# Kernel optimization log

Measured on AMD Instinct MI355X. Metric: run time of the kernel, lower is better.

The kernel has to match this reference:

```python
import jax, jax.numpy as jnp
import numpy as np

B, T, D = 4, 2048, 2048
H = 16
Q_RANK, KV_RANK = 1536, 512
NOPE, ROPE_D, V_D = 128, 64, 128
QK_D = NOPE + ROPE_D  # 192
D_FF = 8192
EPS = 1e-6
THETA = 10000.0
SCALE = QK_D ** -0.5  # mscale = 1 (no rope_scaling)


def _w(key, shape):
    fan_in = shape[0]
    return jax.random.normal(key, shape, dtype=jnp.float32) / np.sqrt(fan_in)


def setup_inputs() -> dict:
    key = jax.random.key(0)
    ks = jax.random.split(key, 16)
    return {
        "x": jax.random.normal(ks[0], (B, T, D), dtype=jnp.float32),
        "ln1_w": jnp.ones((D,), jnp.float32),
        "wq_a": _w(ks[1], (D, Q_RANK)),
        "q_a_ln_w": jnp.ones((Q_RANK,), jnp.float32),
        "wq_b": _w(ks[2], (Q_RANK, H * QK_D)),
        "wkv_a": _w(ks[3], (D, KV_RANK + ROPE_D)),
        "kv_a_ln_w": jnp.ones((KV_RANK,), jnp.float32),
        "wkv_b": _w(ks[4], (KV_RANK, H * (NOPE + V_D))),
        "wo": _w(ks[5], (H * V_D, D)),
        "ln2_w": jnp.ones((D,), jnp.float32),
        "w_gate": _w(ks[6], (D, D_FF)),
        "w_up": _w(ks[7], (D, D_FF)),
        "w_down": _w(ks[8], (D_FF, D)),
        "attention_mask": jnp.ones((B, T), jnp.int32),
        "positions": jnp.broadcast_to(jnp.arange(T, dtype=jnp.int32), (B, T)),
    }


def rmsnorm(x, w):
    return x * jax.lax.rsqrt(jnp.mean(x * x, axis=-1, keepdims=True) + EPS) * w


def apply_rope(x, positions):
    # x: [B, T, h, d], positions: [B, T]
    d = x.shape[-1]
    inv_freq = 1.0 / (THETA ** (jnp.arange(0, d, 2, dtype=jnp.float32) / d))
    ang = positions.astype(jnp.float32)[:, :, None] * inv_freq  # [B,T,d/2]
    cos = jnp.cos(ang)[:, :, None, :]
    sin = jnp.sin(ang)[:, :, None, :]
    x1, x2 = jnp.split(x, 2, axis=-1)
    return jnp.concatenate([x1 * cos - x2 * sin, x2 * cos + x1 * sin], axis=-1)


def reference(x, ln1_w, wq_a, q_a_ln_w, wq_b, wkv_a, kv_a_ln_w, wkv_b, wo,
              ln2_w, w_gate, w_up, w_down, attention_mask, positions):
    # --- MLA attention block ---
    h = rmsnorm(x, ln1_w)
    # low-rank q projection
    q = rmsnorm(h @ wq_a, q_a_ln_w) @ wq_b            # [B,T,H*192]
    q = q.reshape(B, T, H, QK_D)
    q_pass, q_rot = jnp.split(q, [NOPE], axis=-1)
    # compressed kv + shared rope key
    ckv = h @ wkv_a                                    # [B,T,512+64]
    k_c, k_rot = jnp.split(ckv, [KV_RANK], axis=-1)
    k_rot = k_rot.reshape(B, T, 1, ROPE_D)
    kv = rmsnorm(k_c, kv_a_ln_w) @ wkv_b               # [B,T,H*(128+128)]
    kv = kv.reshape(B, T, H, NOPE + V_D)
    k_pass, v = jnp.split(kv, [NOPE], axis=-1)
    # split RoPE on rope dims only
    q_rot = apply_rope(q_rot, positions)
    k_rot = jnp.broadcast_to(apply_rope(k_rot, positions), (B, T, H, ROPE_D))
    qh = jnp.concatenate([q_pass, q_rot], axis=-1)     # [B,T,H,192]
    kh = jnp.concatenate([k_pass, k_rot], axis=-1)     # [B,T,H,192]
    # attention with causal + padding mask (V pad-to-192 then slice is a no-op mathematically)
    scores = jnp.einsum('bqhd,bkhd->bhqk', qh, kh) * SCALE
    causal = jnp.tril(jnp.ones((T, T), bool))
    mask = causal[None, None] & attention_mask[:, None, None, :].astype(bool)
    scores = jnp.where(mask, scores, jnp.finfo(scores.dtype).min)
    attn = jax.nn.softmax(scores, axis=-1)
    o = jnp.einsum('bhqk,bkhd->bqhd', attn, v).reshape(B, T, H * V_D)
    x = x + o @ wo
    # --- MLP block ---
    h2 = rmsnorm(x, ln2_w)
    mlp = (jax.nn.silu(h2 @ w_gate) * (h2 @ w_up)) @ w_down
    return x + mlp
```

## Files before the change

kernel.cpp:

```cpp
#include <hip/hip_runtime.h>

typedef float f32x4 __attribute__((ext_vector_type(4)));
typedef __bf16 bf16x8 __attribute__((ext_vector_type(8)));
typedef unsigned short u16x8 __attribute__((ext_vector_type(8)));
typedef unsigned short u16x4 __attribute__((ext_vector_type(4)));

static __device__ __forceinline__ unsigned short f2b(float f) {
  union { float f; unsigned u; } v; v.f = f;
  unsigned r = v.u + 0x7fffu + ((v.u >> 16) & 1u);
  return (unsigned short)(r >> 16);
}
static __device__ __forceinline__ float b2f(unsigned short s) {
  union { unsigned u; float f; } v; v.u = ((unsigned)s) << 16;
  return v.f;
}
static __device__ __forceinline__ void gload_lds16(const unsigned short* g, unsigned short* l) {
  __builtin_amdgcn_global_load_lds((const __attribute__((address_space(1))) void*)g,
                                   (__attribute__((address_space(3))) void*)l, 16, 0, 0);
}

#define NEG_BIG -3.0e38f

__global__ __launch_bounds__(256) void fill_sentinel(float* __restrict__ out, int n, float v) {
  int i = blockIdx.x * 256 + threadIdx.x;
  if (i < n) out[i] = v;
}

__global__ __launch_bounds__(256) void transpose_convert(const float* __restrict__ in,
                                                         unsigned short* __restrict__ out,
                                                         int K, int N, int in_ld, int row0, int col0,
                                                         float scale) {
  __shared__ float tile[32][33];
  const int k0 = blockIdx.y * 32, n0 = blockIdx.x * 32;
  const int tx = threadIdx.x & 31, ty = threadIdx.x >> 5;
#pragma unroll
  for (int i = 0; i < 32; i += 8) {
    int k = k0 + ty + i, n = n0 + tx;
    tile[ty + i][tx] = (k < K && n < N) ? in[(size_t)(row0 + k) * in_ld + col0 + n] : 0.f;
  }
  __syncthreads();
#pragma unroll
  for (int i = 0; i < 32; i += 8) {
    int n = n0 + ty + i, k = k0 + tx;
    if (n < N && k < K) out[(size_t)n * K + k] = f2b(tile[tx][ty + i] * scale);
  }
}

__global__ __launch_bounds__(256) void rmsnorm_kernel(const float* __restrict__ in,
                                                      const float* __restrict__ w,
                                                      unsigned short* __restrict__ out,
                                                      int ncols, int in_stride, int out_stride) {
  const int row = blockIdx.x;
  const float* rp = in + (size_t)row * in_stride;
  const int n4 = ncols >> 2;
  float4 v[2];
  int nv = 0;
  float ss = 0.f;
  for (int c = threadIdx.x; c < n4; c += 256) {
    float4 xv = reinterpret_cast<const float4*>(rp)[c];
    v[nv++] = xv;
    ss += xv.x * xv.x + xv.y * xv.y + xv.z * xv.z + xv.w * xv.w;
  }
#pragma unroll
  for (int m = 32; m; m >>= 1) ss += __shfl_xor(ss, m);
  __shared__ float red[4];
  if ((threadIdx.x & 63) == 0) red[threadIdx.x >> 6] = ss;
  __syncthreads();
  const float total = red[0] + red[1] + red[2] + red[3];
  const float scale = rsqrtf(total / (float)ncols + 1e-6f);
  nv = 0;
  unsigned short* op = out + (size_t)row * out_stride;
  for (int c = threadIdx.x; c < n4; c += 256) {
    float4 xv = v[nv++];
    float4 wv = reinterpret_cast<const float4*>(w)[c];
    u16x4 o;
    o[0] = f2b(xv.x * scale * wv.x);
    o[1] = f2b(xv.y * scale * wv.y);
    o[2] = f2b(xv.z * scale * wv.z);
    o[3] = f2b(xv.w * scale * wv.w);
    reinterpret_cast<u16x4*>(op)[c] = o;
  }
}

__global__ __launch_bounds__(256) void rmsnorm_b16(const unsigned short* __restrict__ in,
                                                   const float* __restrict__ w,
                                                   unsigned short* __restrict__ out,
                                                   int ncols) {
  const int row = blockIdx.x;
  const unsigned short* rp = in + (size_t)row * ncols;
  const int n4 = ncols >> 2;
  float4 v[2];
  int nv = 0;
  float ss = 0.f;
  for (int c = threadIdx.x; c < n4; c += 256) {
    u16x4 xb = reinterpret_cast<const u16x4*>(rp)[c];
    float4 xv = make_float4(b2f(xb[0]), b2f(xb[1]), b2f(xb[2]), b2f(xb[3]));
    v[nv++] = xv;
    ss += xv.x * xv.x + xv.y * xv.y + xv.z * xv.z + xv.w * xv.w;
  }
#pragma unroll
  for (int m = 32; m; m >>= 1) ss += __shfl_xor(ss, m);
  __shared__ float red[4];
  if ((threadIdx.x & 63) == 0) red[threadIdx.x >> 6] = ss;
  __syncthreads();
  const float total = red[0] + red[1] + red[2] + red[3];
  const float scale = rsqrtf(total / (float)ncols + 1e-6f);
  nv = 0;
  unsigned short* op = out + (size_t)row * ncols;
  for (int c = threadIdx.x; c < n4; c += 256) {
    float4 xv = v[nv++];
    float4 wv = reinterpret_cast<const float4*>(w)[c];
    u16x4 o;
    o[0] = f2b(xv.x * scale * wv.x);
    o[1] = f2b(xv.y * scale * wv.y);
    o[2] = f2b(xv.z * scale * wv.z);
    o[3] = f2b(xv.w * scale * wv.w);
    reinterpret_cast<u16x4*>(op)[c] = o;
  }
}

template <int EPI>
__global__ __launch_bounds__(256) void gemm_bt(const unsigned short* __restrict__ A,
                                               const unsigned short* __restrict__ Bt,
                                               float* __restrict__ outf,
                                               unsigned short* __restrict__ outb,
                                               const float* __restrict__ res,
                                               const unsigned short* __restrict__ aux,
                                               int M, int N, int K) {
  __shared__ __align__(16) unsigned short As[128 * 32];
  __shared__ __align__(16) unsigned short Bs[128 * 32];
  const int tid = threadIdx.x;
  const int l = tid & 63;
  const int lr = l & 15, lg = l >> 4;
  const int wr = tid >> 7, wc = (tid >> 6) & 1;

  const int gx = gridDim.x;
  const int nwg = gx * gridDim.y;
  int lin = blockIdx.y * gx + blockIdx.x;
  {
    const int qq = nwg >> 3, rr = nwg & 7;
    const int xcd = lin & 7, idx = lin >> 3;
    lin = (xcd < rr ? xcd * (qq + 1) : rr * (qq + 1) + (xcd - rr) * qq) + idx;
  }
  const int m0 = (lin / gx) * 128, n0 = (lin % gx) * 128;

  f32x4 acc[4][4] = {};

  for (int k0 = 0; k0 < K; k0 += 32) {
#pragma unroll
    for (int j = 0; j < 2; ++j) {
      const int chunk = j * 256 + tid;
      const int row = chunk >> 2, kc = chunk & 3;
      const unsigned short* ga = A + (size_t)(m0 + row) * K + k0 + kc * 8;
      gload_lds16(ga, &As[(size_t)(j * 256 + (tid & 192)) * 8]);
      int rb = n0 + row;
      if (rb > N - 1) rb = N - 1;
      const unsigned short* gb = Bt + (size_t)rb * K + k0 + kc * 8;
      gload_lds16(gb, &Bs[(size_t)(j * 256 + (tid & 192)) * 8]);
    }
    __syncthreads();
    bf16x8 af[4], bfr[4];
#pragma unroll
    for (int mi = 0; mi < 4; ++mi)
      af[mi] = *reinterpret_cast<const bf16x8*>(&As[(wr * 64 + mi * 16 + lr) * 32 + lg * 8]);
#pragma unroll
    for (int ni = 0; ni < 4; ++ni)
      bfr[ni] = *reinterpret_cast<const bf16x8*>(&Bs[(wc * 64 + ni * 16 + lr) * 32 + lg * 8]);
#pragma unroll
    for (int mi = 0; mi < 4; ++mi)
#pragma unroll
      for (int ni = 0; ni < 4; ++ni)
        acc[mi][ni] = __builtin_amdgcn_mfma_f32_16x16x32_bf16(af[mi], bfr[ni], acc[mi][ni], 0, 0, 0);
    __syncthreads();
  }

#pragma unroll
  for (int mi = 0; mi < 4; ++mi) {
#pragma unroll
    for (int ni = 0; ni < 4; ++ni) {
      const int r0 = m0 + wr * 64 + mi * 16 + lg * 4;
      const int c = n0 + wc * 64 + ni * 16 + lr;
      if (c < N) {
#pragma unroll
        for (int j = 0; j < 4; ++j) {
          const size_t idx = (size_t)(r0 + j) * N + c;
          const float v = acc[mi][ni][j];
          if constexpr (EPI == 0) outf[idx] = v;
          else if constexpr (EPI == 1) outb[idx] = f2b(v);
          else if constexpr (EPI == 2) outf[idx] = v + res[idx];
          else if constexpr (EPI == 3) outb[idx] = f2b(v / (1.f + __expf(-v)));
          else outb[idx] = f2b(v * b2f(aux[idx]));
        }
      }
    }
  }
}

template <int EPI>
__global__ __launch_bounds__(512, 1) void gemm256(const unsigned short* __restrict__ A,
                                                  const unsigned short* __restrict__ Bt,
                                                  float* __restrict__ outf,
                                                  unsigned short* __restrict__ outb,
                                                  const float* __restrict__ res,
                                                  const unsigned short* __restrict__ aux,
                                                  int M, int N, int K) {
  __shared__ __align__(16) unsigned short Lds[2][2][2][128 * 64];
  const int tid = threadIdx.x;
  const int l = tid & 63, lr = l & 15, lg = l >> 4;
  const int w = tid >> 6, swr = w >> 2, swn = w & 3;

  const int gn = N >> 8;
  int lin = blockIdx.x;
  {
    const int nwg = gridDim.x;
    lin = (lin & 7) * (nwg >> 3) + (lin >> 3);
  }
  const int npg = gn << 3;
  const int gid = lin / npg;
  const int idx = lin - gid * npg;
  const int m0 = (gid * 8 + (idx & 7)) * 256;
  const int n0 = (idx >> 3) * 256;

  const int NT = K >> 6;

  f32x4 acc[4][8] = {};

  auto stageh = [&](int mat, int rh, int t) {
    const unsigned short* src = mat ? Bt : A;
    const int rbase = (mat ? n0 : m0) + rh * 128;
    const int d = t & 1;
#pragma unroll
    for (int g = 0; g < 2; ++g) {
      const int c = g * 512 + tid;
      const int row = c >> 3;
      const int kc = (c & 7) ^ (row & 7);
      gload_lds16(src + (size_t)(rbase + row) * K + t * 64 + kc * 8,
                  &Lds[d][mat][rh][(size_t)(g * 512 + (tid & ~63)) * 8]);
    }
  };

  stageh(0, 0, 0); stageh(1, 0, 0); stageh(0, 1, 0); stageh(1, 1, 0);
  if (NT > 1) {
    stageh(0, 0, 1); stageh(1, 0, 1);
    asm volatile("s_waitcnt vmcnt(4)" ::: "memory");
  } else {
    asm volatile("s_waitcnt vmcnt(0)" ::: "memory");
  }
  __builtin_amdgcn_s_barrier();
  __builtin_amdgcn_sched_barrier(0);

#define RD_A(qr, fi, kk)                                                                    \
  af[fi][kk] = *reinterpret_cast<const bf16x8*>(                                            \
      &Lds[d][0][qr][(swr * 64 + (fi) * 16 + lr) * 64 + (((kk) * 4 + lg) ^ (lr & 7)) * 8])
#define RD_B(qc, fj, kk)                                                                    \
  bfv[fj][kk] = *reinterpret_cast<const bf16x8*>(                                           \
      &Lds[d][1][qc][(swn * 32 + (fj) * 16 + lr) * 64 + (((kk) * 4 + lg) ^ (lr & 7)) * 8])
#define MFMAQ(q)                                                                            \
  _Pragma("unroll") for (int fi = 0; fi < 4; ++fi)                                          \
  _Pragma("unroll") for (int fj = 0; fj < 2; ++fj)                                          \
  _Pragma("unroll") for (int kk = 0; kk < 2; ++kk)                                          \
      acc[q][fi * 2 + fj] =                                                                 \
          __builtin_amdgcn_mfma_f32_16x16x32_bf16(af[fi][kk], bfv[fj][kk], acc[q][fi * 2 + fj], 0, 0, 0)

  for (int T = 0; T < NT; ++T) {
    const int d = T & 1;
    bf16x8 af[4][2], bfv[2][2];

    RD_A(0, 0, 0); RD_A(0, 0, 1); RD_A(0, 1, 0); RD_A(0, 1, 1);
    RD_A(0, 2, 0); RD_A(0, 2, 1); RD_A(0, 3, 0); RD_A(0, 3, 1);
    RD_B(0, 0, 0); RD_B(0, 0, 1); RD_B(0, 1, 0); RD_B(0, 1, 1);
    if (T + 1 < NT) stageh(0, 1, T + 1);
    __builtin_amdgcn_s_setprio(1);
    MFMAQ(0);
    __builtin_amdgcn_s_setprio(0);
    if (T + 1 < NT) asm volatile("s_waitcnt vmcnt(6)" ::: "memory");
    else            asm volatile("s_waitcnt vmcnt(0)" ::: "memory");
    __builtin_amdgcn_s_barrier();
    __builtin_amdgcn_sched_barrier(0);

    RD_B(1, 0, 0); RD_B(1, 0, 1); RD_B(1, 1, 0); RD_B(1, 1, 1);
    if (T + 1 < NT) stageh(1, 1, T + 1);
    __builtin_amdgcn_s_setprio(1);
    MFMAQ(1);
    __builtin_amdgcn_s_setprio(0);
    __builtin_amdgcn_s_barrier();
    __builtin_amdgcn_sched_barrier(0);

    RD_A(1, 0, 0); RD_A(1, 0, 1); RD_A(1, 1, 0); RD_A(1, 1, 1);
    RD_A(1, 2, 0); RD_A(1, 2, 1); RD_A(1, 3, 0); RD_A(1, 3, 1);
    RD_B(0, 0, 0); RD_B(0, 0, 1); RD_B(0, 1, 0); RD_B(0, 1, 1);
    if (T + 2 < NT) stageh(0, 0, T + 2);
    __builtin_amdgcn_s_setprio(1);
    MFMAQ(2);
    __builtin_amdgcn_s_setprio(0);
    __builtin_amdgcn_s_barrier();
    __builtin_amdgcn_sched_barrier(0);

    RD_B(1, 0, 0); RD_B(1, 0, 1); RD_B(1, 1, 0); RD_B(1, 1, 1);
    if (T + 2 < NT) stageh(1, 0, T + 2);
    __builtin_amdgcn_s_setprio(1);
    MFMAQ(3);
    __builtin_amdgcn_s_setprio(0);
    if (T + 2 < NT)      asm volatile("s_waitcnt vmcnt(8)" ::: "memory");
    else if (T + 1 < NT) asm volatile("s_waitcnt vmcnt(4)" ::: "memory");
    __builtin_amdgcn_s_barrier();
    __builtin_amdgcn_sched_barrier(0);
  }

#undef RD_A
#undef RD_B
#undef MFMAQ

#pragma unroll
  for (int q = 0; q < 4; ++q) {
    const int qr = q >> 1, qc = q & 1;
#pragma unroll
    for (int fi = 0; fi < 4; ++fi) {
#pragma unroll
      for (int fj = 0; fj < 2; ++fj) {
        const int r = m0 + qr * 128 + swr * 64 + fi * 16 + lg * 4;
        const int c = n0 + qc * 128 + swn * 32 + fj * 16 + lr;
#pragma unroll
        for (int j = 0; j < 4; ++j) {
          const size_t idx2 = (size_t)(r + j) * N + c;
          const float v = acc[q][fi * 2 + fj][j];
          if constexpr (EPI == 0) outf[idx2] = v;
          else if constexpr (EPI == 1) outb[idx2] = f2b(v);
          else if constexpr (EPI == 2) outf[idx2] = v + res[idx2];
          else if constexpr (EPI == 3) outb[idx2] = f2b(v / (1.f + __expf(-v)));
          else outb[idx2] = f2b(v * b2f(aux[idx2]));
        }
      }
    }
  }
}

__global__ __launch_bounds__(256) void rope_q(unsigned short* __restrict__ q,
                                              const int* __restrict__ positions) {
  const int row = blockIdx.x;
  const int pos = positions[row];
  unsigned short* qp = q + (size_t)row * 3072;
  const int tid = threadIdx.x;
#pragma unroll
  for (int i = 0; i < 2; ++i) {
    int e = i * 256 + tid;
    int hh = e >> 5, j = e & 31;
    int base = hh * 192 + 128;
    float x1 = b2f(qp[base + j]), x2 = b2f(qp[base + 32 + j]);
    float freq = __expf(-(float)j * (9.210340371976184f / 32.f));
    float sa, ca;
    __sincosf((float)pos * freq, &sa, &ca);
    qp[base + j] = f2b(x1 * ca - x2 * sa);
    qp[base + 32 + j] = f2b(x2 * ca + x1 * sa);
  }
}

__global__ __launch_bounds__(256) void repack_k(const unsigned short* __restrict__ kv,
                                                const float* __restrict__ ckv,
                                                const int* __restrict__ positions,
                                                unsigned short* __restrict__ kh) {
  const int row = blockIdx.x;
  const int tid = threadIdx.x;
  {
    const int hh = tid >> 4, db = tid & 15;
    u16x8 v = *reinterpret_cast<const u16x8*>(kv + (size_t)row * 4096 + hh * 256 + db * 8);
    *reinterpret_cast<u16x8*>(kh + (size_t)row * 3072 + hh * 192 + db * 8) = v;
  }
  __shared__ float o1[32], o2[32];
  if (tid < 32) {
    const int j = tid;
    float x1 = ckv[(size_t)row * 576 + 512 + j];
    float x2 = ckv[(size_t)row * 576 + 544 + j];
    const int pos = positions[row];
    float freq = __expf(-(float)j * (9.210340371976184f / 32.f));
    float sa, ca;
    __sincosf((float)pos * freq, &sa, &ca);
    o1[j] = x1 * ca - x2 * sa;
    o2[j] = x2 * ca + x1 * sa;
  }
  __syncthreads();
#pragma unroll
  for (int i = 0; i < 4; ++i) {
    int e = i * 256 + tid;
    int hh = e >> 6, d = e & 63;
    float v = (d < 32) ? o1[d] : o2[d - 32];
    kh[(size_t)row * 3072 + hh * 192 + 128 + d] = f2b(v);
  }
}

__global__ __launch_bounds__(512) void mla_attn(const unsigned short* __restrict__ qh,
                                                const unsigned short* __restrict__ kh,
                                                const unsigned short* __restrict__ kv,
                                                unsigned short* __restrict__ o) {
  const int T = 2048, H = 16;
  const int bx = blockIdx.x;
  const int b = blockIdx.y >> 4;
  const int h = blockIdx.y & 15;
  const int tid = threadIdx.x, w = tid >> 6, l = tid & 63;
  const int lg = l >> 4, lr = l & 15;

  __shared__ __align__(16) unsigned short Ks[64 * 200];
  __shared__ __align__(16) unsigned short Vts[128 * 64];
  __shared__ __align__(16) unsigned short Pl[8][16 * 72];
  __shared__ float exs[8][16];

  int krow[3], kcol[3];
#pragma unroll
  for (int i = 0; i < 3; ++i) { int c = i * 512 + tid; krow[i] = c / 24; kcol[i] = (c % 24) * 8; }
  const int vkvp = tid >> 4;
  const int vf0 = (tid & 15) * 8;

  const unsigned short* kbase0 = kh + (((size_t)b * T) * H + h) * 192;
  const unsigned short* vbase0 = kv + (((size_t)b * T) * H + h) * 256 + 128;

  bf16x8 ones;
#pragma unroll
  for (int e = 0; e < 8; ++e) ones[e] = (__bf16)1.0f;

  for (int half = 0; half < 2; ++half) {
    const int qt = half ? (15 - bx) : bx;

    bf16x8 qa[6];
    {
      const size_t qrow = (size_t)b * T + qt * 128 + w * 16 + lr;
      const unsigned short* qp = qh + (qrow * H + h) * 192 + lg * 8;
#pragma unroll
      for (int kc = 0; kc < 6; ++kc)
        qa[kc] = *reinterpret_cast<const bf16x8*>(qp + kc * 32);
    }

    u16x8 kreg[3], vregA, vregB;
#pragma unroll
    for (int i = 0; i < 3; ++i)
      kreg[i] = *reinterpret_cast<const u16x8*>(kbase0 + (size_t)krow[i] * 3072 + kcol[i]);
    vregA = *reinterpret_cast<const u16x8*>(vbase0 + (size_t)(2 * vkvp) * 4096 + vf0);
    vregB = *reinterpret_cast<const u16x8*>(vbase0 + (size_t)(2 * vkvp + 1) * 4096 + vf0);

    f32x4 ot[8] = {};
    f32x4 lacc = {};
    float mrow[4] = {NEG_BIG, NEG_BIG, NEG_BIG, NEG_BIG};

    const int ktmax = 2 * qt + 1;
    for (int kt = 0; kt <= ktmax; ++kt) {
#pragma unroll
      for (int i = 0; i < 3; ++i)
        *reinterpret_cast<u16x8*>(&Ks[krow[i] * 200 + kcol[i]]) = kreg[i];
      {
        const int c7 = (vf0 >> 3) & 7;
#pragma unroll
        for (int e = 0; e < 8; ++e) {
          const int blk = (vkvp >> 2) ^ (e ^ c7);
          const unsigned val = (unsigned)(unsigned short)vregA[e] |
                               ((unsigned)(unsigned short)vregB[e] << 16);
          *reinterpret_cast<unsigned*>(&Vts[(vf0 + e) * 64 + blk * 8 + (vkvp & 3) * 2]) = val;
        }
      }
      __syncthreads();

      if (kt < ktmax) {
        const unsigned short* kb = kbase0 + (size_t)(kt + 1) * 64 * 3072;
        const unsigned short* vb = vbase0 + (size_t)(kt + 1) * 64 * 4096;
#pragma unroll
        for (int i = 0; i < 3; ++i)
          kreg[i] = *reinterpret_cast<const u16x8*>(kb + (size_t)krow[i] * 3072 + kcol[i]);
        vregA = *reinterpret_cast<const u16x8*>(vb + (size_t)(2 * vkvp) * 4096 + vf0);
        vregB = *reinterpret_cast<const u16x8*>(vb + (size_t)(2 * vkvp + 1) * 4096 + vf0);
      }

      f32x4 s4[4];
#pragma unroll
      for (int ni = 0; ni < 4; ++ni) {
        f32x4 a = {};
#pragma unroll
        for (int kc = 0; kc < 6; ++kc) {
          bf16x8 kf = *reinterpret_cast<const bf16x8*>(&Ks[(ni * 16 + lr) * 200 + kc * 32 + lg * 8]);
          a = __builtin_amdgcn_mfma_f32_16x16x32_bf16(qa[kc], kf, a, 0, 0, 0);
        }
        s4[ni] = a;
      }
      if (kt >= 2 * qt) {
#pragma unroll
        for (int ni = 0; ni < 4; ++ni) {
          const int colr = ni * 16 + lr;
#pragma unroll
          for (int j = 0; j < 4; ++j) {
            const int qrl = qt * 128 + w * 16 + lg * 4 + j - kt * 64;
            if (colr > qrl) s4[ni][j] = NEG_BIG;
          }
        }
      }

      float pmj[4];
      int need = 0;
#pragma unroll
      for (int j = 0; j < 4; ++j) {
        pmj[j] = fmaxf(fmaxf(s4[0][j], s4[1][j]), fmaxf(s4[2][j], s4[3][j]));
        need |= (pmj[j] > mrow[j] + 8.f) ? 1 : 0;
      }
      if (__any(need)) {
        float al[4];
#pragma unroll
        for (int j = 0; j < 4; ++j) {
          float rm = pmj[j];
#pragma unroll
          for (int m = 1; m < 16; m <<= 1) rm = fmaxf(rm, __shfl_xor(rm, m));
          const float mn = fmaxf(mrow[j], rm);
          al[j] = __expf(mrow[j] - mn);
          mrow[j] = mn;
        }
        if (lr == 0) {
#pragma unroll
          for (int j = 0; j < 4; ++j) exs[w][lg * 4 + j] = al[j];
        }
        const float af = exs[w][lr];
#pragma unroll
        for (int mi = 0; mi < 8; ++mi) {
          ot[mi][0] *= af; ot[mi][1] *= af; ot[mi][2] *= af; ot[mi][3] *= af;
        }
        lacc[0] *= af; lacc[1] *= af; lacc[2] *= af; lacc[3] *= af;
      }

#pragma unroll
      for (int ni = 0; ni < 4; ++ni)
#pragma unroll
        for (int j = 0; j < 4; ++j)
          Pl[w][(lg * 4 + j) * 72 + ni * 16 + lr] = f2b(__expf(s4[ni][j] - mrow[j]));

      bf16x8 pf0 = *reinterpret_cast<const bf16x8*>(&Pl[w][lr * 72 + lg * 8]);
      bf16x8 pf1 = *reinterpret_cast<const bf16x8*>(&Pl[w][lr * 72 + 32 + lg * 8]);
      lacc = __builtin_amdgcn_mfma_f32_16x16x32_bf16(ones, pf0, lacc, 0, 0, 0);
      lacc = __builtin_amdgcn_mfma_f32_16x16x32_bf16(ones, pf1, lacc, 0, 0, 0);
#pragma unroll
      for (int mi = 0; mi < 8; ++mi) {
        const int f = mi * 16 + lr;
        const int sfz = (f & 7) ^ ((f >> 3) & 7);
        const int blk0 = lg ^ sfz;
        const int blk1 = (4 + lg) ^ sfz;
        bf16x8 vf0r = *reinterpret_cast<const bf16x8*>(&Vts[f * 64 + blk0 * 8]);
        ot[mi] = __builtin_amdgcn_mfma_f32_16x16x32_bf16(vf0r, pf0, ot[mi], 0, 0, 0);
        bf16x8 vf1r = *reinterpret_cast<const bf16x8*>(&Vts[f * 64 + blk1 * 8]);
        ot[mi] = __builtin_amdgcn_mfma_f32_16x16x32_bf16(vf1r, pf1, ot[mi], 0, 0, 0);
      }
      __syncthreads();
    }

    const float li = 1.f / lacc[0];
    const size_t orow = (size_t)b * T + qt * 128 + w * 16 + lr;
#pragma unroll
    for (int mi = 0; mi < 8; ++mi)
#pragma unroll
      for (int j = 0; j < 4; ++j) {
        const int feat = mi * 16 + lg * 4 + j;
        o[orow * 2048 + h * 128 + feat] = f2b(ot[mi][j] * li);
      }
  }
}

extern "C" void kernel_launch(void* const* d_in, const int* in_sizes, int n_in,
                              void* d_out, int out_size, void* d_ws, size_t ws_size,
                              hipStream_t stream) {
  (void)in_sizes; (void)n_in;
  const float* x      = (const float*)d_in[0];
  const float* ln1_w  = (const float*)d_in[1];
  const float* wq_a   = (const float*)d_in[2];
  const float* qaln_w = (const float*)d_in[3];
  const float* wq_b   = (const float*)d_in[4];
  const float* wkv_a  = (const float*)d_in[5];
  const float* kvln_w = (const float*)d_in[6];
  const float* wkv_b  = (const float*)d_in[7];
  const float* wo     = (const float*)d_in[8];
  const float* ln2_w  = (const float*)d_in[9];
  const float* w_gate = (const float*)d_in[10];
  const float* w_up   = (const float*)d_in[11];
  const float* w_down = (const float*)d_in[12];
  const int*   pos    = (const int*)d_in[14];
  float* out = (float*)d_out;

  const int Mt = 8192;

  char* ws = (char*)d_ws;
  const size_t R1 = 0;
  const size_t R2 = R1 + 67108864;
  const size_t R3 = R2 + 50331648;
  const size_t R4 = R3 + 50331648;
  const size_t R5 = R4 + 33554432;
  const size_t R6 = R5 + 18874368;
  const size_t REQ = R6 + 9437184;

  if (ws_size < REQ) {
    fill_sentinel<<<dim3((out_size + 255) / 256), dim3(256), 0, stream>>>(
        out, out_size, (float)(ws_size >> 20));
    return;
  }

  unsigned short* qa_b16 = (unsigned short*)(ws + R1);
  unsigned short* kvbuf  = (unsigned short*)(ws + R1);
  unsigned short* qbuf   = (unsigned short*)(ws + R2);
  unsigned short* qan    = (unsigned short*)(ws + R3);
  unsigned short* ckvn   = (unsigned short*)(ws + R3);
  unsigned short* khbuf  = (unsigned short*)(ws + R3);
  unsigned short* hbuf   = (unsigned short*)(ws + R4);
  unsigned short* obuf   = (unsigned short*)(ws + R4);
  float*          ckv    = (float*)(ws + R5);
  unsigned short* slotW  = (unsigned short*)(ws + R6);
  unsigned short* actb  = (unsigned short*)(ws + 0);
  unsigned short* h2b   = (unsigned short*)(ws + 134217728);
  unsigned short* wsl2  = (unsigned short*)(ws + 167772160);

  dim3 blk(256);
  dim3 blk5(512);
  auto tcf = [&](const float* W, int K, int N, float scale) {
    transpose_convert<<<dim3((N + 31) / 32, (K + 31) / 32), blk, 0, stream>>>(W, slotW, K, N, N, 0, 0, scale);
  };
  auto g256 = [&](auto epi, const unsigned short* Aa, const unsigned short* Bb, float* of,
                  unsigned short* ob, const float* rs, const unsigned short* ax, int N, int K) {
    gemm256<decltype(epi)::value><<<dim3(32 * (N >> 8)), blk5, 0, stream>>>(Aa, Bb, of, ob, rs, ax, Mt, N, K);
  };

  rmsnorm_kernel<<<Mt, blk, 0, stream>>>(x, ln1_w, hbuf, 2048, 2048, 2048);
  tcf(wq_a, 2048, 1536, 1.0f);
  g256(std::integral_constant<int,1>{}, hbuf, slotW, nullptr, qa_b16, nullptr, nullptr, 1536, 2048);
  rmsnorm_b16<<<Mt, blk, 0, stream>>>(qa_b16, qaln_w, qan, 1536);
  tcf(wq_b, 1536, 3072, 0.07216878364870322f);
  g256(std::integral_constant<int,1>{}, qan, slotW, nullptr, qbuf, nullptr, nullptr, 3072, 1536);
  tcf(wkv_a, 2048, 576, 1.0f);
  gemm_bt<0><<<dim3(5, 64), blk, 0, stream>>>(hbuf, slotW, ckv, nullptr, nullptr, nullptr, Mt, 576, 2048);
  rmsnorm_kernel<<<Mt, blk, 0, stream>>>(ckv, kvln_w, ckvn, 512, 576, 512);
  tcf(wkv_b, 512, 4096, 1.0f);
  g256(std::integral_constant<int,1>{}, ckvn, slotW, nullptr, kvbuf, nullptr, nullptr, 4096, 512);
  rope_q<<<Mt, blk, 0, stream>>>(qbuf, pos);
  repack_k<<<Mt, blk, 0, stream>>>(kvbuf, ckv, pos, khbuf);
  mla_attn<<<dim3(8, 64), blk5, 0, stream>>>(qbuf, khbuf, kvbuf, obuf);
  tcf(wo, 2048, 2048, 1.0f);
  g256(std::integral_constant<int,2>{}, obuf, slotW, out, nullptr, x, nullptr, 2048, 2048);
  rmsnorm_kernel<<<Mt, blk, 0, stream>>>(out, ln2_w, h2b, 2048, 2048, 2048);
  transpose_convert<<<dim3(256, 64), blk, 0, stream>>>(w_gate, wsl2, 2048, 8192, 8192, 0, 0, 1.0f);
  g256(std::integral_constant<int,3>{}, h2b, wsl2, nullptr, actb, nullptr, nullptr, 8192, 2048);
  transpose_convert<<<dim3(256, 64), blk, 0, stream>>>(w_up, wsl2, 2048, 8192, 8192, 0, 0, 1.0f);
  g256(std::integral_constant<int,4>{}, h2b, wsl2, nullptr, actb, nullptr, actb, 8192, 2048);
  transpose_convert<<<dim3(64, 256), blk, 0, stream>>>(w_down, wsl2, 8192, 2048, 2048, 0, 0, 1.0f);
  g256(std::integral_constant<int,2>{}, actb, wsl2, out, nullptr, out, nullptr, 2048, 8192);
}
```

Before: 1.486 ms.

## Fuse gate and up GEMMs via interleaved weights with SiLU-mul epilogue

```diff
diff --git a/kernel.cpp b/kernel.cpp
--- a/kernel.cpp
+++ b/kernel.cpp
@@ -29,7 +29,7 @@
 __global__ __launch_bounds__(256) void transpose_convert(const float* __restrict__ in,
                                                          unsigned short* __restrict__ out,
                                                          int K, int N, int in_ld, int row0, int col0,
-                                                         float scale) {
+                                                         float scale, int ilv_off) {
   __shared__ float tile[32][33];
   const int k0 = blockIdx.y * 32, n0 = blockIdx.x * 32;
   const int tx = threadIdx.x & 31, ty = threadIdx.x >> 5;
@@ -42,7 +42,10 @@
 #pragma unroll
   for (int i = 0; i < 32; i += 8) {
     int n = n0 + ty + i, k = k0 + tx;
-    if (n < N && k < K) out[(size_t)n * K + k] = f2b(tile[tx][ty + i] * scale);
+    if (n < N && k < K) {
+      const int orow = (ilv_off >= 0) ? (((n >> 7) << 8) + (n & 127) + ilv_off) : n;
+      out[(size_t)orow * K + k] = f2b(tile[tx][ty + i] * scale);
+    }
   }
 }
 
@@ -311,24 +314,45 @@
 #undef RD_B
 #undef MFMAQ
 
-#pragma unroll
-  for (int q = 0; q < 4; ++q) {
-    const int qr = q >> 1, qc = q & 1;
-#pragma unroll
-    for (int fi = 0; fi < 4; ++fi) {
-#pragma unroll
-      for (int fj = 0; fj < 2; ++fj) {
-        const int r = m0 + qr * 128 + swr * 64 + fi * 16 + lg * 4;
-        const int c = n0 + qc * 128 + swn * 32 + fj * 16 + lr;
-#pragma unroll
-        for (int j = 0; j < 4; ++j) {
-          const size_t idx2 = (size_t)(r + j) * N + c;
-          const float v = acc[q][fi * 2 + fj][j];
-          if constexpr (EPI == 0) outf[idx2] = v;
-          else if constexpr (EPI == 1) outb[idx2] = f2b(v);
-          else if constexpr (EPI == 2) outf[idx2] = v + res[idx2];
-          else if constexpr (EPI == 3) outb[idx2] = f2b(v / (1.f + __expf(-v)));
-          else outb[idx2] = f2b(v * b2f(aux[idx2]));
+  if constexpr (EPI == 5) {
+    const int actN = N >> 1;
+#pragma unroll
+    for (int qr = 0; qr < 2; ++qr) {
+#pragma unroll
+      for (int fi = 0; fi < 4; ++fi) {
+#pragma unroll
+        for (int fj = 0; fj < 2; ++fj) {
+          const int r0 = m0 + qr * 128 + swr * 64 + fi * 16 + lg * 4;
+          const int cA = (n0 >> 1) + swn * 32 + fj * 16 + lr;
+#pragma unroll
+          for (int j = 0; j < 4; ++j) {
+            const float g = acc[qr * 2][fi * 2 + fj][j];
+            const float u = acc[qr * 2 + 1][fi * 2 + fj][j];
+            outb[(size_t)(r0 + j) * actN + cA] = f2b(g / (1.f + __expf(-g)) * u);
+          }
+        }
+      }
+    }
+  } else {
+#pragma unroll
+    for (int q = 0; q < 4; ++q) {
+      const int qr = q >> 1, qc = q & 1;
+#pragma unroll
+      for (int fi = 0; fi < 4; ++fi) {
+#pragma unroll
+        for (int fj = 0; fj < 2; ++fj) {
+          const int r = m0 + qr * 128 + swr * 64 + fi * 16 + lg * 4;
+          const int c = n0 + qc * 128 + swn * 32 + fj * 16 + lr;
+#pragma unroll
+          for (int j = 0; j < 4; ++j) {
+            const size_t idx2 = (size_t)(r + j) * N + c;
+            const float v = acc[q][fi * 2 + fj][j];
+            if constexpr (EPI == 0) outf[idx2] = v;
+            else if constexpr (EPI == 1) outb[idx2] = f2b(v);
+            else if constexpr (EPI == 2) outf[idx2] = v + res[idx2];
+            else if constexpr (EPI == 3) outb[idx2] = f2b(v / (1.f + __expf(-v)));
+            else if constexpr (EPI == 4) outb[idx2] = f2b(v * b2f(aux[idx2]));
+          }
         }
       }
     }
@@ -610,7 +634,7 @@
   dim3 blk(256);
   dim3 blk5(512);
   auto tcf = [&](const float* W, int K, int N, float scale) {
-    transpose_convert<<<dim3((N + 31) / 32, (K + 31) / 32), blk, 0, stream>>>(W, slotW, K, N, N, 0, 0, scale);
+    transpose_convert<<<dim3((N + 31) / 32, (K + 31) / 32), blk, 0, stream>>>(W, slotW, K, N, N, 0, 0, scale, -1);
   };
   auto g256 = [&](auto epi, const unsigned short* Aa, const unsigned short* Bb, float* of,
                   unsigned short* ob, const float* rs, const unsigned short* ax, int N, int K) {
@@ -634,10 +658,11 @@
   tcf(wo, 2048, 2048, 1.0f);
   g256(std::integral_constant<int,2>{}, obuf, slotW, out, nullptr, x, nullptr, 2048, 2048);
   rmsnorm_kernel<<<Mt, blk, 0, stream>>>(out, ln2_w, h2b, 2048, 2048, 2048);
-  transpose_convert<<<dim3(256, 64), blk, 0, stream>>>(w_gate, wsl2, 2048, 8192, 8192, 0, 0, 1.0f);
-  g256(std::integral_constant<int,3>{}, h2b, wsl2, nullptr, actb, nullptr, nullptr, 8192, 2048);
-  transpose_convert<<<dim3(256, 64), blk, 0, stream>>>(w_up, wsl2, 2048, 8192, 8192, 0, 0, 1.0f);
-  g256(std::integral_constant<int,4>{}, h2b, wsl2, nullptr, actb, nullptr, actb, 8192, 2048);
-  transpose_convert<<<dim3(64, 256), blk, 0, stream>>>(w_down, wsl2, 8192, 2048, 2048, 0, 0, 1.0f);
-  g256(std::integral_constant<int,2>{}, actb, wsl2, out, nullptr, out, nullptr, 2048, 8192);
-}
+  for (int c = 0; c < 2; ++c) {
+    transpose_convert<<<dim3(128, 64), blk, 0, stream>>>(w_gate, wsl2, 2048, 4096, 8192, 0, c * 4096, 1.0f, 0);
+    transpose_convert<<<dim3(128, 64), blk, 0, stream>>>(w_up,   wsl2, 2048, 4096, 8192, 0, c * 4096, 1.0f, 128);
+    g256(std::integral_constant<int,5>{}, h2b, wsl2, nullptr, actb, nullptr, nullptr, 8192, 2048);
+    transpose_convert<<<dim3(64, 128), blk, 0, stream>>>(w_down, wsl2, 4096, 2048, 2048, c * 4096, 0, 1.0f, -1);
+    g256(std::integral_constant<int,2>{}, actb, wsl2, out, nullptr, out, nullptr, 2048, 4096);
+  }
+}
```

After: 1.457 ms, median of 2. No clear change (-2.0%).
